# Performance work log

Hardware: AMD Instinct MI355X
Metric: run time of the kernel (lower is better)

## Reference

```python
import jax, jax.numpy as jnp
import numpy as np
from jax import lax

KS = 16          # kernel_size
VAR_WEIGHT = 1.0
VAR_BIAS = 0.1


def setup_inputs() -> dict:
    key = jax.random.key(0)
    k1, k2 = jax.random.split(key)
    N1, N2, C, W, H = 128, 128, 512, 16, 16
    x = jax.random.normal(k1, (N1, C, W, H), dtype=jnp.float32)
    y = jax.random.normal(k2, (N2, C, W, H), dtype=jnp.float32)
    # Conv2d buffer: box kernel scaled by var_weight / kernel_size**2
    kernel = jnp.ones((1, 1, KS, KS), dtype=jnp.float32) * (VAR_WEIGHT / KS ** 2)
    return {"x": x, "y": y, "kernel": kernel}


def _box_conv(patch, kernel):
    # patch: [N, 1, W, H]; padding=0, stride=1, dilation=1 -> VALID, full-spatial
    out = lax.conv_general_dilated(
        patch, kernel,
        window_strides=(1, 1), padding="VALID",
        dimension_numbers=("NCHW", "OIHW", "NCHW"))
    return out + VAR_BIAS


def reference(x, y, kernel):
    N1, C, W, H = x.shape
    N2 = y.shape[0]
    # Fused correlation volume: mean over channels of the outer product,
    # computed as a batched GEMM per spatial location (no N1*N2*C*W*H blowup).
    xy = jnp.einsum("icwh,jcwh->ijwh", x, y) / C          # [N1, N2, W, H]
    xy = xy.reshape(N1 * N2, 1, W, H)
    # Box-filter conv collapses spatial dims (kernel_size == W == H, padding=0).
    r = _box_conv(xy, kernel)                              # [N1*N2, 1, 1, 1]
    # Note: original also convolves xx/yy, but NonlinKP(final_kp).xy only
    # uses the xy branch for the returned value.
    return r.reshape(N1, N2)
```

## Files before the change

kernel.cpp:

```cpp
#include <hip/hip_runtime.h>
#include <hip/hip_bf16.h>

typedef short s16x8 __attribute__((ext_vector_type(8)));
typedef float f32x4 __attribute__((ext_vector_type(4)));

#define M_DIM   128
#define K_DIM   131072
#define NSPLIT  512
#define KC      (K_DIM / NSPLIT)
#define BK      64
#define NSTEP   (KC / BK)
#define THREADS 512
#define OUT_N   (M_DIM * M_DIM)

__device__ __forceinline__ unsigned short f2bf(float f) {
    unsigned u = __builtin_bit_cast(unsigned, f);
    u += 0x7fffu + ((u >> 16) & 1u);
    return (unsigned short)(u >> 16);
}
__device__ __forceinline__ float bf2f(unsigned short h) {
    unsigned u = ((unsigned)h) << 16;
    return __builtin_bit_cast(float, u);
}
__device__ __forceinline__ s16x8 cvt8(float4 a, float4 b) {
    s16x8 r;
    r[0] = (short)f2bf(a.x); r[1] = (short)f2bf(a.y);
    r[2] = (short)f2bf(a.z); r[3] = (short)f2bf(a.w);
    r[4] = (short)f2bf(b.x); r[5] = (short)f2bf(b.y);
    r[6] = (short)f2bf(b.z); r[7] = (short)f2bf(b.w);
    return r;
}

__global__ __launch_bounds__(THREADS) void gemm_splitk(
    const float* __restrict__ x, const float* __restrict__ y,
    const float* __restrict__ kern,
    unsigned short* __restrict__ ws, float* __restrict__ out, int use_ws)
{
    __shared__ __align__(16) short lds[2][2][M_DIM][BK];

    const int t    = threadIdx.x;
    const long kb0 = (long)blockIdx.x * KC;

    const int srow = t >> 3;
    const int sg   = t & 7;
    const int wofs = (sg ^ (srow & 7)) * 8;

    const float* xa = x + (size_t)srow        * K_DIM + kb0 + sg * 8;
    const float* xb = x + (size_t)(srow + 64) * K_DIM + kb0 + sg * 8;
    const float* ya = y + (size_t)srow        * K_DIM + kb0 + sg * 8;
    const float* yb = y + (size_t)(srow + 64) * K_DIM + kb0 + sg * 8;

    const int wave = t >> 6;
    const int lane = t & 63;
    const int wr   = wave >> 2;
    const int wc   = wave & 3;
    const int l15  = lane & 15;
    const int l4   = lane >> 4;

    f32x4 acc[4][2] = {};
    float4 A0,A1,A2,A3,A4,A5,A6,A7;
    float4 B0,B1,B2,B3,B4,B5,B6,B7;

    #define STAGE_LOAD(R, kb)                                            \
        R##0 = *(const float4*)(xa + (kb)); R##1 = *(const float4*)(xa + (kb) + 4); \
        R##2 = *(const float4*)(xb + (kb)); R##3 = *(const float4*)(xb + (kb) + 4); \
        R##4 = *(const float4*)(ya + (kb)); R##5 = *(const float4*)(ya + (kb) + 4); \
        R##6 = *(const float4*)(yb + (kb)); R##7 = *(const float4*)(yb + (kb) + 4);

    #define STAGE_WRITE(R, buf)                                          \
        *(s16x8*)&lds[buf][0][srow     ][wofs] = cvt8(R##0, R##1);       \
        *(s16x8*)&lds[buf][0][srow + 64][wofs] = cvt8(R##2, R##3);       \
        *(s16x8*)&lds[buf][1][srow     ][wofs] = cvt8(R##4, R##5);       \
        *(s16x8*)&lds[buf][1][srow + 64][wofs] = cvt8(R##6, R##7);

    auto compute = [&](int buf) {
        #pragma unroll
        for (int ks = 0; ks < 2; ++ks) {
            s16x8 af[4], bf[2];
            const int g = ks * 4 + l4;
            #pragma unroll
            for (int m = 0; m < 4; ++m) {
                const int row = wr * 64 + m * 16 + l15;
                af[m] = *(const s16x8*)&lds[buf][0][row][(g ^ (row & 7)) * 8];
            }
            #pragma unroll
            for (int n = 0; n < 2; ++n) {
                const int row = wc * 32 + n * 16 + l15;
                bf[n] = *(const s16x8*)&lds[buf][1][row][(g ^ (row & 7)) * 8];
            }
            #pragma unroll
            for (int m = 0; m < 4; ++m)
                #pragma unroll
                for (int n = 0; n < 2; ++n)
                    acc[m][n] = __builtin_amdgcn_mfma_f32_16x16x32_bf16(
                        af[m], bf[n], acc[m][n], 0, 0, 0);
        }
    };

    STAGE_LOAD(A, 0)
    STAGE_LOAD(B, BK)
    STAGE_WRITE(A, 0)
    __syncthreads();

    #pragma unroll
    for (int s = 0; s < NSTEP; s += 2) {
        if (s + 2 < NSTEP) { STAGE_LOAD(A, (long)(s + 2) * BK) }
        compute(0);
        STAGE_WRITE(B, 1)
        __syncthreads();
        if (s + 3 < NSTEP) { STAGE_LOAD(B, (long)(s + 3) * BK) }
        compute(1);
        if (s + 2 < NSTEP) { STAGE_WRITE(A, 0) }
        __syncthreads();
    }

    if (use_ws) {
        unsigned short* wp = ws + (size_t)blockIdx.x * OUT_N;
        #pragma unroll
        for (int m = 0; m < 4; ++m) {
            const int row = wr * 64 + m * 16 + l4 * 4;
            #pragma unroll
            for (int n = 0; n < 2; ++n) {
                const int col = wc * 32 + n * 16 + l15;
                #pragma unroll
                for (int r = 0; r < 4; ++r)
                    wp[(size_t)(row + r) * M_DIM + col] =
                        (unsigned short)f2bf(acc[m][n][r]);
            }
        }
    } else {
        const float scale = kern[0] * (1.0f / 512.0f);
        #pragma unroll
        for (int m = 0; m < 4; ++m) {
            const int row = wr * 64 + m * 16 + l4 * 4;
            #pragma unroll
            for (int n = 0; n < 2; ++n) {
                const int col = wc * 32 + n * 16 + l15;
                #pragma unroll
                for (int r = 0; r < 4; ++r)
                    atomicAdd(out + (size_t)(row + r) * M_DIM + col,
                              acc[m][n][r] * scale);
            }
        }
    }
    #undef STAGE_LOAD
    #undef STAGE_WRITE
}

__global__ __launch_bounds__(256) void reduce_k(
    const unsigned short* __restrict__ ws, const float* __restrict__ kern,
    float* __restrict__ out)
{
    __shared__ float red[16][16][4];
    const int b  = blockIdx.x;
    const int qi = threadIdx.x & 15;
    const int sc = threadIdx.x >> 4;
    const int e0 = b * 64 + qi * 4;

    float a0 = 0.f, a1 = 0.f, a2 = 0.f, a3 = 0.f;
    #pragma unroll 4
    for (int s = sc * 32; s < sc * 32 + 32; ++s) {
        ushort4 v = *(const ushort4*)(ws + (size_t)s * OUT_N + e0);
        a0 += bf2f(v.x); a1 += bf2f(v.y); a2 += bf2f(v.z); a3 += bf2f(v.w);
    }
    red[sc][qi][0] = a0; red[sc][qi][1] = a1;
    red[sc][qi][2] = a2; red[sc][qi][3] = a3;
    __syncthreads();
    for (int off = 8; off > 0; off >>= 1) {
        if (sc < off) {
            #pragma unroll
            for (int r = 0; r < 4; ++r)
                red[sc][qi][r] += red[sc + off][qi][r];
        }
        __syncthreads();
    }
    if (sc == 0) {
        const float scale = kern[0] * (1.0f / 512.0f);
        float4 o;
        o.x = red[0][qi][0] * scale + 0.1f;
        o.y = red[0][qi][1] * scale + 0.1f;
        o.z = red[0][qi][2] * scale + 0.1f;
        o.w = red[0][qi][3] * scale + 0.1f;
        *(float4*)(out + e0) = o;
    }
}

__global__ __launch_bounds__(256) void init_k(float* __restrict__ out) {
    out[blockIdx.x * 256 + threadIdx.x] = 0.1f;
}

extern "C" void kernel_launch(void* const* d_in, const int* in_sizes, int n_in,
                              void* d_out, int out_size, void* d_ws, size_t ws_size,
                              hipStream_t stream) {
    const float* x    = (const float*)d_in[0];
    const float* y    = (const float*)d_in[1];
    const float* kern = (const float*)d_in[2];
    float* out = (float*)d_out;

    const size_t need = (size_t)NSPLIT * OUT_N * sizeof(unsigned short);
    if (ws_size >= need && d_ws != nullptr) {
        unsigned short* ws = (unsigned short*)d_ws;
        gemm_splitk<<<NSPLIT, THREADS, 0, stream>>>(x, y, kern, ws, out, 1);
        reduce_k<<<256, 256, 0, stream>>>(ws, kern, out);
    } else {
        init_k<<<OUT_N / 256, 256, 0, stream>>>(out);
        gemm_splitk<<<NSPLIT, THREADS, 0, stream>>>(x, y, kern, nullptr, out, 0);
    }
}
```

Measured before the change: 32.96 us.

## Halve split-K count and store partials in fragment-native packed layout

Split-K count drops from 512 to 256 blocks, so each block does twice as much K and the workspace traffic is halved. Partial results are now packed as bf16 pairs and written as one coalesced uint4 per thread per m-fragment, in the MFMA register layout, replacing scattered 2-byte stores. The reduce kernel reads this layout with 16-byte loads and maps indices back to output coordinates with index arithmetic. The cost is fewer blocks than the 256 CUs can comfortably hide latency with, and less parallelism in the GEMM stage.

Result: faster. 29.16 us (-11.5%).

```diff
diff --git a/kernel.cpp b/kernel.cpp
--- a/kernel.cpp
+++ b/kernel.cpp
@@ -6,12 +6,13 @@
 
 #define M_DIM   128
 #define K_DIM   131072
-#define NSPLIT  512
+#define NSPLIT  256
 #define KC      (K_DIM / NSPLIT)
 #define BK      64
 #define NSTEP   (KC / BK)
 #define THREADS 512
 #define OUT_N   (M_DIM * M_DIM)
+#define WS_U32_PER_BLK 8192
 
 __device__ __forceinline__ unsigned short f2bf(float f) {
     unsigned u = __builtin_bit_cast(unsigned, f);
@@ -34,7 +35,7 @@
 __global__ __launch_bounds__(THREADS) void gemm_splitk(
     const float* __restrict__ x, const float* __restrict__ y,
     const float* __restrict__ kern,
-    unsigned short* __restrict__ ws, float* __restrict__ out, int use_ws)
+    unsigned int* __restrict__ ws32, float* __restrict__ out, int use_ws)
 {
     __shared__ __align__(16) short lds[2][2][M_DIM][BK];
 
@@ -115,18 +116,15 @@
     }
 
     if (use_ws) {
-        unsigned short* wp = ws + (size_t)blockIdx.x * OUT_N;
+        uint4* wp4 = (uint4*)(ws32 + (size_t)blockIdx.x * WS_U32_PER_BLK);
         #pragma unroll
         for (int m = 0; m < 4; ++m) {
-            const int row = wr * 64 + m * 16 + l4 * 4;
-            #pragma unroll
-            for (int n = 0; n < 2; ++n) {
-                const int col = wc * 32 + n * 16 + l15;
-                #pragma unroll
-                for (int r = 0; r < 4; ++r)
-                    wp[(size_t)(row + r) * M_DIM + col] =
-                        (unsigned short)f2bf(acc[m][n][r]);
-            }
+            uint4 v;
+            v.x = (unsigned)f2bf(acc[m][0][0]) | ((unsigned)f2bf(acc[m][0][1]) << 16);
+            v.y = (unsigned)f2bf(acc[m][0][2]) | ((unsigned)f2bf(acc[m][0][3]) << 16);
+            v.z = (unsigned)f2bf(acc[m][1][0]) | ((unsigned)f2bf(acc[m][1][1]) << 16);
+            v.w = (unsigned)f2bf(acc[m][1][2]) | ((unsigned)f2bf(acc[m][1][3]) << 16);
+            wp4[m * 512 + t] = v;
         }
     } else {
         const float scale = kern[0] * (1.0f / 512.0f);
@@ -148,40 +146,56 @@
 }
 
 __global__ __launch_bounds__(256) void reduce_k(
-    const unsigned short* __restrict__ ws, const float* __restrict__ kern,
+    const unsigned int* __restrict__ ws32, const float* __restrict__ kern,
     float* __restrict__ out)
 {
-    __shared__ float red[16][16][4];
-    const int b  = blockIdx.x;
-    const int qi = threadIdx.x & 15;
-    const int sc = threadIdx.x >> 4;
-    const int e0 = b * 64 + qi * 4;
-
-    float a0 = 0.f, a1 = 0.f, a2 = 0.f, a3 = 0.f;
-    #pragma unroll 4
-    for (int s = sc * 32; s < sc * 32 + 32; ++s) {
-        ushort4 v = *(const ushort4*)(ws + (size_t)s * OUT_N + e0);
-        a0 += bf2f(v.x); a1 += bf2f(v.y); a2 += bf2f(v.z); a3 += bf2f(v.w);
-    }
-    red[sc][qi][0] = a0; red[sc][qi][1] = a1;
-    red[sc][qi][2] = a2; red[sc][qi][3] = a3;
+    __shared__ float red[32][8][8];
+    const int rb = blockIdx.x;
+    const int t  = threadIdx.x;
+    const int qi = t & 7;
+    const int sc = t >> 3;
+
+    const uint4* rp = (const uint4*)(ws32 + (size_t)(sc * 8) * WS_U32_PER_BLK
+                                          + rb * 32 + qi * 4);
+    float a[8] = {};
+    #pragma unroll
+    for (int j = 0; j < 8; ++j) {
+        uint4 v = rp[(size_t)j * (WS_U32_PER_BLK / 4)];
+        a[0] += bf2f((unsigned short)(v.x & 0xffff));
+        a[1] += bf2f((unsigned short)(v.x >> 16));
+        a[2] += bf2f((unsigned short)(v.y & 0xffff));
+        a[3] += bf2f((unsigned short)(v.y >> 16));
+        a[4] += bf2f((unsigned short)(v.z & 0xffff));
+        a[5] += bf2f((unsigned short)(v.z >> 16));
+        a[6] += bf2f((unsigned short)(v.w & 0xffff));
+        a[7] += bf2f((unsigned short)(v.w >> 16));
+    }
+    #pragma unroll
+    for (int i = 0; i < 8; ++i) red[sc][qi][i] = a[i];
     __syncthreads();
-    for (int off = 8; off > 0; off >>= 1) {
+    for (int off = 16; off > 0; off >>= 1) {
         if (sc < off) {
             #pragma unroll
-            for (int r = 0; r < 4; ++r)
-                red[sc][qi][r] += red[sc + off][qi][r];
+            for (int i = 0; i < 8; ++i)
+                red[sc][qi][i] += red[sc + off][qi][i];
         }
         __syncthreads();
     }
-    if (sc == 0) {
+    if (t < 64) {
+        const int j    = rb * 32 + (t >> 1);
+        const int half = t & 1;
+        const int w    = j & 3;
+        const int gt   = (j >> 2) & 511;
+        const int c    = j >> 11;
+        const int m_   = c;
+        const int n_   = w >> 1;
+        const int rp_  = w & 1;
+        const int wv   = gt >> 6, ln = gt & 63;
+        const int row  = (wv >> 2) * 64 + m_ * 16 + (ln >> 4) * 4 + rp_ * 2 + half;
+        const int col  = (wv & 3) * 32 + n_ * 16 + (ln & 15);
         const float scale = kern[0] * (1.0f / 512.0f);
-        float4 o;
-        o.x = red[0][qi][0] * scale + 0.1f;
-        o.y = red[0][qi][1] * scale + 0.1f;
-        o.z = red[0][qi][2] * scale + 0.1f;
-        o.w = red[0][qi][3] * scale + 0.1f;
-        *(float4*)(out + e0) = o;
+        const float v = red[0][t >> 3][((t >> 1) & 3) * 2 + half];
+        out[row * M_DIM + col] = v * scale + 0.1f;
     }
 }
 
@@ -197,11 +211,11 @@
     const float* kern = (const float*)d_in[2];
     float* out = (float*)d_out;
 
-    const size_t need = (size_t)NSPLIT * OUT_N * sizeof(unsigned short);
+    const size_t need = (size_t)NSPLIT * WS_U32_PER_BLK * 4;
     if (ws_size >= need && d_ws != nullptr) {
-        unsigned short* ws = (unsigned short*)d_ws;
-        gemm_splitk<<<NSPLIT, THREADS, 0, stream>>>(x, y, kern, ws, out, 1);
-        reduce_k<<<256, 256, 0, stream>>>(ws, kern, out);
+        unsigned int* ws32 = (unsigned int*)d_ws;
+        gemm_splitk<<<NSPLIT, THREADS, 0, stream>>>(x, y, kern, ws32, out, 1);
+        reduce_k<<<256, 256, 0, stream>>>(ws32, kern, out);
     } else {
         init_k<<<OUT_N / 256, 256, 0, stream>>>(out);
         gemm_splitk<<<NSPLIT, THREADS, 0, stream>>>(x, y, kern, nullptr, out, 0);
```
